# Kernel optimization log

Hardware: AMD Instinct MI355X
Metric: run time of the kernel (lower is better)

The kernel has to match this reference:

```python
import jax, jax.numpy as jnp
import numpy as np

N_WIRES = 8
DIM = 2 ** N_WIRES  # 256
N_OPS = 20

# Fixed realization of tq.RandomLayer(n_ops=20): ops drawn once with a fixed seed.
_rs = np.random.RandomState(0)
RAND_OPS = []
for _ in range(N_OPS):
    k = int(_rs.randint(4))
    if k == 3:
        c, t = _rs.choice(N_WIRES, 2, replace=False)
        RAND_OPS.append(("cnot", int(c), int(t)))
    else:
        RAND_OPS.append((("rx", "ry", "rz")[k], int(_rs.randint(N_WIRES)), 0))

_idx = np.arange(DIM)
# Z eigenvalue sign per wire per basis state (wire 0 = most significant bit)
ZSIGN_NP = np.stack([1.0 - 2.0 * ((_idx >> (N_WIRES - 1 - w)) & 1) for w in range(N_WIRES)]).astype(np.float32)
ZSIGN = jnp.asarray(ZSIGN_NP)        # [8, 256]
ZS_T = jnp.asarray(ZSIGN_NP.T)       # [256, 8]

# CNOT is a basis permutation: precompute index maps for each cnot op.
PERMS = {}
for _i, _op in enumerate(RAND_OPS):
    if _op[0] == "cnot":
        _c, _t = _op[1], _op[2]
        _cb = (_idx >> (N_WIRES - 1 - _c)) & 1
        PERMS[_i] = jnp.asarray(_idx ^ (_cb << (N_WIRES - 1 - _t)))


def _ry_mat(t):
    c = jnp.cos(t * 0.5).astype(jnp.complex64)
    s = jnp.sin(t * 0.5).astype(jnp.complex64)
    return jnp.stack([jnp.stack([c, -s]), jnp.stack([s, c])])


def _rx_mat(t):
    c = jnp.cos(t * 0.5).astype(jnp.complex64)
    s = (-1j * jnp.sin(t * 0.5)).astype(jnp.complex64)
    return jnp.stack([jnp.stack([c, s]), jnp.stack([s, c])])


def _apply_1q(state, U, w):
    # state: [B, 256]; apply 2x2 U on wire w
    B = state.shape[0]
    s = state.reshape(B, 2 ** w, 2, -1)
    return jnp.einsum('ij,bajc->baic', U, s).reshape(B, DIM)


def _forward(x, ry_theta, rand_params, W1, b1, W2, b2):
    B, S, E = x.shape
    f = x.reshape(B * S, E)[:, :N_WIRES]  # encoder uses input_idx 0..7
    # Encoder: RY(f_w) on |0> for each wire -> product state, built by kron chain
    c = jnp.cos(f * 0.5)
    s = jnp.sin(f * 0.5)
    state = jnp.ones((B * S, 1), jnp.float32)
    for w in range(N_WIRES):
        v = jnp.stack([c[:, w], s[:, w]], axis=-1)  # [BS, 2]
        state = (state[:, :, None] * v[:, None, :]).reshape(B * S, -1)
    state = state.astype(jnp.complex64)  # [BS, 256]
    # Fixed random layer
    for i, op in enumerate(RAND_OPS):
        kind = op[0]
        if kind == "cnot":
            state = state[:, PERMS[i]]
        elif kind == "rz":
            ph = jnp.exp((-0.5j * rand_params[i]) * ZSIGN[op[1]]).astype(jnp.complex64)
            state = state * ph[None, :]
        elif kind == "rx":
            state = _apply_1q(state, _rx_mat(rand_params[i]), op[1])
        else:
            state = _apply_1q(state, _ry_mat(rand_params[i]), op[1])
    # Trainable per-wire RY gates
    for w in range(N_WIRES):
        state = _apply_1q(state, _ry_mat(ry_theta[w]), w)
    # MeasureAll(PauliZ): <Z_w> = sum_b |amp_b|^2 * zsign_w(b)
    probs = (state.real ** 2 + state.imag ** 2)  # [BS, 256] float32
    expv = probs @ ZS_T                          # [BS, 8]
    h = jax.nn.relu(expv @ W1.T + b1)
    out = h @ W2.T + b2
    return out.reshape(B, S, -1)


def setup_inputs() -> dict:
    key = jax.random.key(0)
    k1, k2, k3, k4, k5 = jax.random.split(key, 5)
    B, S, E = 4, 4096, 512
    pi = 3.14159265
    x = jax.random.normal(k1, (B, S, E), jnp.float32)
    ry_theta = jax.random.uniform(k2, (N_WIRES,), jnp.float32, -pi, pi)
    rand_params = jax.random.uniform(k3, (N_OPS,), jnp.float32, -pi, pi)
    W1 = jax.random.normal(k4, (64, N_WIRES), jnp.float32) * (1.0 / np.sqrt(N_WIRES))
    b1 = jnp.zeros((64,), jnp.float32)
    W2 = jax.random.normal(k5, (E, 64), jnp.float32) * (1.0 / 8.0)
    b2 = jnp.zeros((E,), jnp.float32)
    return {"x": x, "ry_theta": ry_theta, "rand_params": rand_params, "W1": W1, "b1": b1, "W2": W2, "b2": b2}


def reference(x, ry_theta, rand_params, W1, b1, W2, b2):
    return _forward(x, ry_theta, rand_params, W1, b1, W2, b2)
```

## Files before the change

kernel.cpp:

```cpp
#include <hip/hip_runtime.h>
#include <hip/hip_fp16.h>
#include <cstdint>

#define N_RAND   20
#define N_GATES  28
#define E_DIM    512

struct OpsArg { int d[N_GATES]; };

struct MT19937ce {
  uint32_t mt[624] = {};
  int mti = 0;
  constexpr void seed(uint32_t s){
    mt[0]=s;
    for(int i=1;i<624;i++) mt[i]=1812433253u*(mt[i-1]^(mt[i-1]>>30))+(uint32_t)i;
    mti=624;
  }
  constexpr uint32_t next(){
    if(mti>=624){
      for(int i=0;i<624;i++){
        uint32_t y=(mt[i]&0x80000000u)|(mt[(i+1)%624]&0x7fffffffu);
        mt[i]=mt[(i+397)%624]^(y>>1)^((y&1u)?0x9908b0dfu:0u);
      }
      mti=0;
    }
    uint32_t y=mt[mti++];
    y^=y>>11; y^=(y<<7)&0x9d2c5680u; y^=(y<<15)&0xefc60000u; y^=y>>18;
    return y;
  }
  constexpr uint32_t interval(uint32_t mx){
    if(!mx) return 0;
    uint32_t mask=mx; mask|=mask>>1; mask|=mask>>2; mask|=mask>>4; mask|=mask>>8; mask|=mask>>16;
    uint32_t v = next()&mask;
    while(v>mx) v = next()&mask;
    return v;
  }
};

constexpr OpsArg build_ops_ce(){
  MT19937ce rs; rs.seed(0);
  OpsArg o{};
  for(int i=0;i<N_RAND;i++){
    uint32_t k = rs.interval(3);
    if(k==3){
      int perm[8] = {0,1,2,3,4,5,6,7};
      for(int j=7;j>=1;j--){
        uint32_t t=rs.interval((uint32_t)j);
        int tmp=perm[j]; perm[j]=perm[t]; perm[t]=tmp;
      }
      o.d[i] = 3 | (perm[0]<<2) | (perm[1]<<5);
    } else {
      uint32_t w = rs.interval(7);
      o.d[i] = (int)k | ((int)w<<2);
    }
  }
  for(int i=0;i<8;i++) o.d[N_RAND+i] = 1 | (i<<2);
  return o;
}
inline constexpr OpsArg OPS = build_ops_ce();

__device__ __forceinline__ float readlane_f(float v, int l){
  return __int_as_float(__builtin_amdgcn_readlane(__float_as_int(v), l));
}
template<int CTRL>
__device__ __forceinline__ float dpp_mov(float v){
  int s = __float_as_int(v);
  return __int_as_float(__builtin_amdgcn_update_dpp(s, s, CTRL, 0xF, 0xF, false));
}
template<int M>
__device__ __forceinline__ float xl(float v){
  if constexpr (M==1)      return dpp_mov<0xB1>(v);
  else if constexpr (M==2) return dpp_mov<0x4E>(v);
  else return __int_as_float(__builtin_amdgcn_ds_swizzle(__float_as_int(v), (M<<10)|0x1F));
}
template<int L>
__device__ __forceinline__ float bcast(float v){
  return __int_as_float(__builtin_amdgcn_ds_swizzle(__float_as_int(v), L<<5));
}

typedef _Float16 v2h __attribute__((ext_vector_type(2)));
typedef _Float16 v8h __attribute__((ext_vector_type(8)));
typedef float    v4f __attribute__((ext_vector_type(4)));
union HU  { uint32_t u; v2h h; };

template<int G>
__device__ __forceinline__ void run_gates(float (&ar)[8], float (&ai)[8],
                                          const float (&sgn)[5], int l,
                                          float cv, float sv)
{
  if constexpr (G < N_GATES){
    constexpr int dd   = OPS.d[G];
    constexpr int kind = dd & 3;
    constexpr int wa   = (dd>>2) & 7;
    constexpr int wb   = (dd>>5) & 7;
    const float gc = readlane_f(cv, G);
    const float gs = readlane_f(sv, G);

    if constexpr (kind == 3){
      if constexpr (wa < 3 && wb < 3){
        constexpr int Rc = 4>>wa, Rt = 4>>wb;
        #pragma unroll
        for (int r=0;r<8;r++){
          if ((r & Rc) && !(r & Rt)){
            float t0=ar[r]; ar[r]=ar[r|Rt]; ar[r|Rt]=t0;
            float t1=ai[r]; ai[r]=ai[r|Rt]; ai[r|Rt]=t1;
          }
        }
      } else if constexpr (wa < 3){
        constexpr int Rc = 4>>wa, Mt = 16>>(wb-3);
        #pragma unroll
        for (int r=0;r<8;r++){
          if (r & Rc){ ar[r]=xl<Mt>(ar[r]); ai[r]=xl<Mt>(ai[r]); }
        }
      } else if constexpr (wb < 3){
        constexpr int Mc = 16>>(wa-3), Rt = 4>>wb;
        const bool cb = (l & Mc) != 0;
        #pragma unroll
        for (int r=0;r<8;r++){
          if (!(r & Rt)){
            float alo=ar[r], ahi=ar[r|Rt];
            ar[r]    = cb ? ahi : alo;  ar[r|Rt] = cb ? alo : ahi;
            float blo=ai[r], bhi=ai[r|Rt];
            ai[r]    = cb ? bhi : blo;  ai[r|Rt] = cb ? blo : bhi;
          }
        }
      } else {
        constexpr int Mc = 16>>(wa-3), Mt = 16>>(wb-3);
        const bool cb = (l & Mc) != 0;
        #pragma unroll
        for (int r=0;r<8;r++){
          float pr = xl<Mt>(ar[r]), pi_ = xl<Mt>(ai[r]);
          ar[r] = cb ? pr  : ar[r];
          ai[r] = cb ? pi_ : ai[r];
        }
      }
    } else if constexpr (kind == 2){
      if constexpr (wa < 3){
        constexpr int Rb = 4>>wa;
        #pragma unroll
        for (int r=0;r<8;r++){
          const float pim = (r & Rb) ? gs : -gs;
          float nr = gc*ar[r] - pim*ai[r];
          ai[r] = gc*ai[r] + pim*ar[r];
          ar[r] = nr;
        }
      } else {
        constexpr int SI = wa-3;
        const float pim = sgn[SI]*gs;
        #pragma unroll
        for (int r=0;r<8;r++){
          float nr = gc*ar[r] - pim*ai[r];
          ai[r] = gc*ai[r] + pim*ar[r];
          ar[r] = nr;
        }
      }
    } else if constexpr (kind == 1){
      if constexpr (wa < 3){
        constexpr int Rb = 4>>wa;
        #pragma unroll
        for (int r=0;r<8;r++){
          if (!(r & Rb)){
            const int h = r|Rb;
            float lr=ar[r], li=ai[r], hr=ar[h], hii=ai[h];
            ar[r]=gc*lr - gs*hr;  ai[r]=gc*li - gs*hii;
            ar[h]=gs*lr + gc*hr;  ai[h]=gs*li + gc*hii;
          }
        }
      } else {
        constexpr int M = 16>>(wa-3), SI = wa-3;
        const float sg = sgn[SI]*gs;
        #pragma unroll
        for (int r=0;r<8;r++){
          float pr = xl<M>(ar[r]), pi_ = xl<M>(ai[r]);
          ar[r] = gc*ar[r] + sg*pr;
          ai[r] = gc*ai[r] + sg*pi_;
        }
      }
    } else {
      if constexpr (wa < 3){
        constexpr int Rb = 4>>wa;
        #pragma unroll
        for (int r=0;r<8;r++){
          if (!(r & Rb)){
            const int h = r|Rb;
            float lr=ar[r], li=ai[r], hr=ar[h], hii=ai[h];
            ar[r]=gc*lr + gs*hii;  ai[r]=gc*li - gs*hr;
            ar[h]=gc*hr + gs*li;   ai[h]=gc*hii - gs*lr;
          }
        }
      } else {
        constexpr int M = 16>>(wa-3);
        #pragma unroll
        for (int r=0;r<8;r++){
          float pr = xl<M>(ar[r]), pi_ = xl<M>(ai[r]);
          ar[r] = gc*ar[r] + gs*pi_;
          ai[r] = gc*ai[r] - gs*pr;
        }
      }
    }
    run_gates<G+1>(ar, ai, sgn, l, cv, sv);
  }
}

__global__ __launch_bounds__(256)
void qcirc_kernel(const float* __restrict__ x,
                  const float* __restrict__ ry_theta,
                  const float* __restrict__ rand_params,
                  const float* __restrict__ W1,
                  const float* __restrict__ b1,
                  __half* __restrict__ Hout)
{
  const int tid  = threadIdx.x;
  const int lane = tid & 63;
  const int l    = lane & 31;
  const int wave = tid >> 6;
  const int token = blockIdx.x*8 + wave*2 + (lane>>5);

  float th = 0.f;
  if (lane < N_GATES)
    th = (lane < N_RAND) ? rand_params[lane] : ry_theta[lane - N_RAND];
  float cv, sv;
  __sincosf(0.5f*th, &sv, &cv);

  const float4 xa = *(const float4*)(x + (size_t)token*E_DIM);
  const float4 xb = *(const float4*)(x + (size_t)token*E_DIM + 4);
  float c[8], s[8];
  {
    float xs[8] = {xa.x, xa.y, xa.z, xa.w, xb.x, xb.y, xb.z, xb.w};
    #pragma unroll
    for (int w=0; w<8; ++w) __sincosf(0.5f*xs[w], &s[w], &c[w]);
  }

  float sgn[5];
  sgn[0] = (l&16) ? 1.f : -1.f;
  sgn[1] = (l& 8) ? 1.f : -1.f;
  sgn[2] = (l& 4) ? 1.f : -1.f;
  sgn[3] = (l& 2) ? 1.f : -1.f;
  sgn[4] = (l& 1) ? 1.f : -1.f;

  float lp = ((l&16)? s[3]:c[3]) * ((l&8)? s[4]:c[4]);
  lp *= ((l&4)? s[5]:c[5]) * ((l&2)? s[6]:c[6]);
  lp *= ((l&1)? s[7]:c[7]);
  const float q00=c[0]*c[1], q01=c[0]*s[1], q10=s[0]*c[1], q11=s[0]*s[1];
  const float c2lp=c[2]*lp, s2lp=s[2]*lp;
  float ar[8], ai[8];
  ar[0]=q00*c2lp; ar[1]=q00*s2lp; ar[2]=q01*c2lp; ar[3]=q01*s2lp;
  ar[4]=q10*c2lp; ar[5]=q10*s2lp; ar[6]=q11*c2lp; ar[7]=q11*s2lp;
  #pragma unroll
  for (int r=0;r<8;r++) ai[r]=0.f;

  run_gates<0>(ar, ai, sgn, l, cv, sv);

  float p[8];
  #pragma unroll
  for (int r=0;r<8;r++) p[r] = ar[r]*ar[r] + ai[r]*ai[r];
  const float t1a=p[0]+p[1], t1b=p[2]+p[3], t1c=p[4]+p[5], t1d=p[6]+p[7];
  const float s0a=t1a+t1b, s0b=t1c+t1d;
  float P  = s0a + s0b;
  float e0 = s0a - s0b;
  float e1 = (t1a+t1c) - (t1b+t1d);
  float e2 = (p[0]-p[1])+(p[2]-p[3])+(p[4]-p[5])+(p[6]-p[7]);
  {
    float t;
    t=xl<1>(e0); e0+=t;  t=xl<1>(e1); e1+=t;  t=xl<1>(e2); e2+=t;
    t=xl<1>(P);  P = fmaf(-sgn[4], P, t);
    t=xl<2>(e0); e0+=t;  t=xl<2>(e1); e1+=t;  t=xl<2>(e2); e2+=t;
    t=xl<2>(P);  P = fmaf(-sgn[3], P, t);
    t=xl<4>(e0); e0+=t;  t=xl<4>(e1); e1+=t;  t=xl<4>(e2); e2+=t;
    t=xl<4>(P);  P = fmaf(-sgn[2], P, t);
    t=xl<8>(e0); e0+=t;  t=xl<8>(e1); e1+=t;  t=xl<8>(e2); e2+=t;
    t=xl<8>(P);  P = fmaf(-sgn[1], P, t);
    t=xl<16>(e0); e0+=t; t=xl<16>(e1); e1+=t; t=xl<16>(e2); e2+=t;
    t=xl<16>(P); P = fmaf(-sgn[0], P, t);
  }
  const float e3 = bcast<16>(P);
  const float e4 = bcast<8>(P);
  const float e5 = bcast<4>(P);
  const float e6 = bcast<2>(P);
  const float e7 = bcast<1>(P);

  const float4 wA0 = *(const float4*)(W1 + (size_t)(2*l)*8);
  const float4 wA1 = *(const float4*)(W1 + (size_t)(2*l)*8 + 4);
  const float4 wB0 = *(const float4*)(W1 + (size_t)(2*l+1)*8);
  const float4 wB1 = *(const float4*)(W1 + (size_t)(2*l+1)*8 + 4);
  const float2 bb  = *(const float2*)(b1 + 2*l);
  float h0 = bb.x + wA0.x*e0 + wA0.y*e1 + wA0.z*e2 + wA0.w*e3
                  + wA1.x*e4 + wA1.y*e5 + wA1.z*e6 + wA1.w*e7;
  float h1 = bb.y + wB0.x*e0 + wB0.y*e1 + wB0.z*e2 + wB0.w*e3
                  + wB1.x*e4 + wB1.y*e5 + wB1.z*e6 + wB1.w*e7;
  HU pk;
  pk.h = v2h{(_Float16)fmaxf(h0,0.f), (_Float16)fmaxf(h1,0.f)};
  *(uint32_t*)((char*)Hout + ((size_t)token*64 + 2*l)*2) = pk.u;
}

#define TS_STRIDE 68
__global__ __launch_bounds__(256)
void mlp2_mfma4(const __half* __restrict__ Hh,
                const float* __restrict__ W2,
                const float* __restrict__ b2,
                float* __restrict__ out)
{
  __shared__ float Ts[4][16*TS_STRIDE];

  const int tid  = threadIdx.x;
  const int lane = tid & 63;
  const int wave = tid >> 6;
  const int wid  = blockIdx.x*4 + wave;
  const int mt   = wid >> 3;
  const int ng   = wid & 7;
  const int rr   = lane & 15;
  const int quad = lane >> 4;

  const v8h a0 = *(const v8h*)(Hh + ((size_t)(mt*16 + rr))*64 + quad*8);
  const v8h a1 = *(const v8h*)(Hh + ((size_t)(mt*16 + rr))*64 + 32 + quad*8);

  #pragma unroll
  for (int j=0;j<4;++j){
    const int e = ng*64 + j*16 + rr;
    const float4 wa = *(const float4*)(W2 + (size_t)e*64 + quad*8);
    const float4 wb = *(const float4*)(W2 + (size_t)e*64 + quad*8 + 4);
    const float4 wc = *(const float4*)(W2 + (size_t)e*64 + 32 + quad*8);
    const float4 wd = *(const float4*)(W2 + (size_t)e*64 + 32 + quad*8 + 4);
    const v8h b0 = v8h{(_Float16)wa.x,(_Float16)wa.y,(_Float16)wa.z,(_Float16)wa.w,
                      (_Float16)wb.x,(_Float16)wb.y,(_Float16)wb.z,(_Float16)wb.w};
    const v8h b1 = v8h{(_Float16)wc.x,(_Float16)wc.y,(_Float16)wc.z,(_Float16)wc.w,
                      (_Float16)wd.x,(_Float16)wd.y,(_Float16)wd.z,(_Float16)wd.w};
    v4f acc = {0.f,0.f,0.f,0.f};
    acc = __builtin_amdgcn_mfma_f32_16x16x32_f16(a0, b0, acc, 0, 0, 0);
    acc = __builtin_amdgcn_mfma_f32_16x16x32_f16(a1, b1, acc, 0, 0, 0);
    #pragma unroll
    for (int r2=0;r2<4;r2++)
      Ts[wave][(quad*4+r2)*TS_STRIDE + j*16 + rr] = acc[r2];
  }

  __syncthreads();

  const float4 bias = *(const float4*)(b2 + ng*64 + rr*4);
  #pragma unroll
  for (int k=0;k<4;++k){
    const int row = 4*k + quad;
    float4 v = *(const float4*)&Ts[wave][row*TS_STRIDE + rr*4];
    v.x += bias.x; v.y += bias.y; v.z += bias.z; v.w += bias.w;
    const int t = mt*16 + row;
    *(float4*)(out + (size_t)t*E_DIM + ng*64 + rr*4) = v;
  }
}

extern "C" void kernel_launch(void* const* d_in, const int* in_sizes, int n_in,
                              void* d_out, int out_size, void* d_ws, size_t ws_size,
                              hipStream_t stream)
{
  (void)n_in; (void)out_size; (void)ws_size;
  const int ntok = in_sizes[0] / E_DIM;
  __half* Hh = (__half*)d_ws;

  qcirc_kernel<<<ntok/8, 256, 0, stream>>>(
      (const float*)d_in[0],
      (const float*)d_in[1],
      (const float*)d_in[2],
      (const float*)d_in[3],
      (const float*)d_in[4],
      Hh);

  mlp2_mfma4<<<(ntok/16)*8/4, 256, 0, stream>>>(
      Hh,
      (const float*)d_in[5],
      (const float*)d_in[6],
      (float*)d_out);
}
```

Measured before the change: 121.6 us.

## Fuse quantum circuit kernel and second MLP layer into one kernel

Merges the circuit/first-layer kernel and the MFMA second-layer kernel into a single 512-thread block handling 16 tokens. Each block keeps its hidden activations in shared memory instead of writing them to a workspace and reading them back in a second launch. This removes one kernel launch and the global round trip for the hidden tensor. In exchange, blocks are larger and use more shared memory, which may lower occupancy, and every block now reloads all of W2.

```diff
diff --git a/kernel.cpp b/kernel.cpp
--- a/kernel.cpp
+++ b/kernel.cpp
@@ -202,19 +202,27 @@
   }
 }
 
-__global__ __launch_bounds__(256)
-void qcirc_kernel(const float* __restrict__ x,
-                  const float* __restrict__ ry_theta,
-                  const float* __restrict__ rand_params,
-                  const float* __restrict__ W1,
-                  const float* __restrict__ b1,
-                  __half* __restrict__ Hout)
+#define TS_STRIDE 68
+#define HPAD 72
+__global__ __launch_bounds__(512)
+void qffb_fused(const float* __restrict__ x,
+                const float* __restrict__ ry_theta,
+                const float* __restrict__ rand_params,
+                const float* __restrict__ W1,
+                const float* __restrict__ b1,
+                const float* __restrict__ W2,
+                const float* __restrict__ b2,
+                float* __restrict__ out)
 {
+  __shared__ __half Hs[16][HPAD];
+  __shared__ float  Ts[8][16*TS_STRIDE];
+
   const int tid  = threadIdx.x;
   const int lane = tid & 63;
   const int l    = lane & 31;
   const int wave = tid >> 6;
-  const int token = blockIdx.x*8 + wave*2 + (lane>>5);
+  const int trow = wave*2 + (lane>>5);
+  const int token = blockIdx.x*16 + trow;
 
   float th = 0.f;
   if (lane < N_GATES)
@@ -290,29 +298,17 @@
                   + wB1.x*e4 + wB1.y*e5 + wB1.z*e6 + wB1.w*e7;
   HU pk;
   pk.h = v2h{(_Float16)fmaxf(h0,0.f), (_Float16)fmaxf(h1,0.f)};
-  *(uint32_t*)((char*)Hout + ((size_t)token*64 + 2*l)*2) = pk.u;
-}
-
-#define TS_STRIDE 68
-__global__ __launch_bounds__(256)
-void mlp2_mfma4(const __half* __restrict__ Hh,
-                const float* __restrict__ W2,
-                const float* __restrict__ b2,
-                float* __restrict__ out)
-{
-  __shared__ float Ts[4][16*TS_STRIDE];
-
-  const int tid  = threadIdx.x;
-  const int lane = tid & 63;
-  const int wave = tid >> 6;
-  const int wid  = blockIdx.x*4 + wave;
-  const int mt   = wid >> 3;
-  const int ng   = wid & 7;
+  *(uint32_t*)((char*)&Hs[trow][0] + 4*l) = pk.u;
+
+  __syncthreads();
+
+  const int mt   = blockIdx.x;
+  const int ng   = wave;
   const int rr   = lane & 15;
   const int quad = lane >> 4;
 
-  const v8h a0 = *(const v8h*)(Hh + ((size_t)(mt*16 + rr))*64 + quad*8);
-  const v8h a1 = *(const v8h*)(Hh + ((size_t)(mt*16 + rr))*64 + 32 + quad*8);
+  const v8h a0 = *(const v8h*)&Hs[rr][quad*8];
+  const v8h a1 = *(const v8h*)&Hs[rr][32 + quad*8];
 
   #pragma unroll
   for (int j=0;j<4;++j){
@@ -323,17 +319,16 @@
     const float4 wd = *(const float4*)(W2 + (size_t)e*64 + 32 + quad*8 + 4);
     const v8h b0 = v8h{(_Float16)wa.x,(_Float16)wa.y,(_Float16)wa.z,(_Float16)wa.w,
                       (_Float16)wb.x,(_Float16)wb.y,(_Float16)wb.z,(_Float16)wb.w};
-    const v8h b1 = v8h{(_Float16)wc.x,(_Float16)wc.y,(_Float16)wc.z,(_Float16)wc.w,
+    const v8h b1v = v8h{(_Float16)wc.x,(_Float16)wc.y,(_Float16)wc.z,(_Float16)wc.w,
                       (_Float16)wd.x,(_Float16)wd.y,(_Float16)wd.z,(_Float16)wd.w};
     v4f acc = {0.f,0.f,0.f,0.f};
     acc = __builtin_amdgcn_mfma_f32_16x16x32_f16(a0, b0, acc, 0, 0, 0);
-    acc = __builtin_amdgcn_mfma_f32_16x16x32_f16(a1, b1, acc, 0, 0, 0);
+    acc = __builtin_amdgcn_mfma_f32_16x16x32_f16(a1, b1v, acc, 0, 0, 0);
     #pragma unroll
     for (int r2=0;r2<4;r2++)
       Ts[wave][(quad*4+r2)*TS_STRIDE + j*16 + rr] = acc[r2];
   }
 
-  __syncthreads();
 
   const float4 bias = *(const float4*)(b2 + ng*64 + rr*4);
   #pragma unroll
@@ -350,20 +345,15 @@
                               void* d_out, int out_size, void* d_ws, size_t ws_size,
                               hipStream_t stream)
 {
-  (void)n_in; (void)out_size; (void)ws_size;
+  (void)n_in; (void)out_size; (void)d_ws; (void)ws_size;
   const int ntok = in_sizes[0] / E_DIM;
-  __half* Hh = (__half*)d_ws;
-
-  qcirc_kernel<<<ntok/8, 256, 0, stream>>>(
+
+  qffb_fused<<<ntok/16, 512, 0, stream>>>(
       (const float*)d_in[0],
       (const float*)d_in[1],
       (const float*)d_in[2],
       (const float*)d_in[3],
       (const float*)d_in[4],
-      Hh);
-
-  mlp2_mfma4<<<(ntok/16)*8/4, 256, 0, stream>>>(
-      Hh,
       (const float*)d_in[5],
       (const float*)d_in[6],
       (float*)d_out);
```

Result: faster. 111.5 us (-8.3%).
